# Kernel tuning notes

Measured on AMD Instinct MI355X. Metric: run time of the kernel, lower is better.

Reference implementation:

```python
import jax, jax.numpy as jnp
import numpy as np

N = 100000
E = 1600000
D = 128      # input_dim == hidden_dim
C = 40       # output_dim
L = 3        # num_layers
EPS = 1e-12  # F.normalize eps


def setup_inputs() -> dict:
    key = jax.random.key(0)
    ks = jax.random.split(key, 8)
    x = jax.random.normal(ks[0], (N, D), dtype=jnp.float32)
    edge_index = jax.random.randint(ks[1], (2, E), 0, N, dtype=jnp.int64)
    s = 1.0 / np.sqrt(D)
    # SAGEConv: lin_l (neighbor path, with bias), lin_r (root path, no bias)
    Wl = jax.random.uniform(ks[2], (L, D, D), jnp.float32, -s, s)
    bl = jax.random.uniform(ks[3], (L, D), jnp.float32, -s, s)
    Wr = jax.random.uniform(ks[4], (L, D, D), jnp.float32, -s, s)
    Wlin = jax.random.uniform(ks[5], (C, D), jnp.float32, -s, s)
    blin = jax.random.uniform(ks[6], (C,), jnp.float32, -s, s)
    return {"x": x, "edge_index": edge_index, "Wl": Wl, "bl": bl,
            "Wr": Wr, "Wlin": Wlin, "blin": blin}


def reference(x, edge_index, Wl, bl, Wr, Wlin, blin):
    src, dst = edge_index[0], edge_index[1]
    # in-degree counts for mean aggregation (computed once, reused per layer)
    cnt = jax.ops.segment_sum(jnp.ones((E,), jnp.float32), dst, num_segments=N)
    inv_cnt = (1.0 / jnp.maximum(cnt, 1.0))[:, None]  # [N,1]
    z = x
    for i in range(L):
        msg = z[src]  # gather [E, D]
        agg = jax.ops.segment_sum(msg, dst, num_segments=N) * inv_cnt  # mean [N, D]
        out = agg @ Wl[i].T + bl[i] + z @ Wr[i].T
        # SAGEConv normalize=True: L2 normalize per node
        nrm = jnp.linalg.norm(out, axis=-1, keepdims=True)
        out = out / jnp.maximum(nrm, EPS)
        z = jax.nn.relu(out)  # dropout p=0 -> identity
    return z @ Wlin.T + blin  # [N, C]
```

## Files before the change

kernel.cpp:

```cpp
#include <hip/hip_runtime.h>


typedef __bf16 bf16x8 __attribute__((ext_vector_type(8)));
typedef float  f32x4  __attribute__((ext_vector_type(4)));

#define MFMA16(a, b, c) __builtin_amdgcn_mfma_f32_16x16x32_bf16((a), (b), (c), 0, 0, 0)

__device__ __forceinline__ unsigned rne_bf16(float f) {
  unsigned u = __float_as_uint(f);
  unsigned r = u + 0x7FFFu + ((u >> 16) & 1u);
  return r >> 16;
}

__device__ __forceinline__ float bf_lo(unsigned u) { return __uint_as_float(u << 16); }
__device__ __forceinline__ float bf_hi(unsigned u) { return __uint_as_float(u & 0xFFFF0000u); }


__global__ __launch_bounds__(256) void histA_k(const int* __restrict__ dst,
                                               int* __restrict__ ghist, int E) {
  __shared__ int h[128];
  const int tid = threadIdx.x;
  if (tid < 128) h[tid] = 0;
  __syncthreads();
  const int e0 = blockIdx.x * 2048;
#pragma unroll
  for (int j = 0; j < 8; ++j) {
    int e = e0 + j * 256 + tid;
    if (e < E) atomicAdd(&h[dst[e] >> 10], 1);
  }
  __syncthreads();
  if (tid < 128 && h[tid]) atomicAdd(&ghist[tid], h[tid]);
}

__global__ void cscan_k(const int* __restrict__ ghist, int* __restrict__ cbase,
                        int* __restrict__ gcur, int E) {
  __shared__ int sd[128];
  const int tid = threadIdx.x;
  int v = ghist[tid];
  sd[tid] = v;
  __syncthreads();
  for (int off = 1; off < 128; off <<= 1) {
    int u = (tid >= off) ? sd[tid - off] : 0;
    __syncthreads();
    sd[tid] += u;
    __syncthreads();
  }
  int excl = sd[tid] - v;
  cbase[tid] = excl;
  gcur[tid] = excl;
  if (tid == 127) cbase[128] = sd[127];
}

__global__ __launch_bounds__(256) void bucketA_k(
    const int* __restrict__ src, const int* __restrict__ dst,
    int* __restrict__ gcur, unsigned* __restrict__ coarse, int E, int nc) {
  __shared__ int hist[128];
  __shared__ int sd[128];
  __shared__ int lpos[128];
  __shared__ int gbase[128];
  __shared__ unsigned stage[2048];
  __shared__ unsigned char sbuck[2048];

  const int tid = threadIdx.x;
  const int e0 = blockIdx.x * 2048;

  if (tid < 128) hist[tid] = 0;
  __syncthreads();

  int bv[8], pk[8];
#pragma unroll
  for (int j = 0; j < 8; ++j) {
    int e = e0 + j * 256 + tid;
    bv[j] = -1;
    if (e < E) {
      int s = src[e], d = dst[e];
      bv[j] = d >> 10;
      pk[j] = s | ((d & 1023) << 17);
      atomicAdd(&hist[bv[j]], 1);
    }
  }
  __syncthreads();

  if (tid < 128) sd[tid] = hist[tid];
  __syncthreads();
  for (int off = 1; off < 128; off <<= 1) {
    int t = 0;
    if (tid < 128 && tid >= off) t = sd[tid - off];
    __syncthreads();
    if (tid < 128) sd[tid] += t;
    __syncthreads();
  }
  if (tid < 128) {
    int excl = sd[tid] - hist[tid];
    lpos[tid] = excl;
    gbase[tid] = (tid < nc && hist[tid] > 0) ? atomicAdd(&gcur[tid], hist[tid]) : 0;
  }
  __syncthreads();

#pragma unroll
  for (int j = 0; j < 8; ++j) {
    if (bv[j] >= 0) {
      int slot = atomicAdd(&lpos[bv[j]], 1);
      stage[slot] = (unsigned)pk[j];
      sbuck[slot] = (unsigned char)bv[j];
    }
  }
  __syncthreads();

  const int total = sd[127];
  for (int i = tid; i < total; i += 256) {
    int b = sbuck[i];
    int excl = sd[b] - hist[b];
    coarse[gbase[b] + (i - excl)] = stage[i];
  }
}

__global__ __launch_bounds__(256) void bucketB_k(
    const int* __restrict__ cbase, const unsigned* __restrict__ coarse,
    int* __restrict__ esrc, int* __restrict__ offsets,
    float* __restrict__ inv_cnt, int n, int E) {
  __shared__ int hcnt[1024];
  __shared__ int cur[1024];
  __shared__ int sd[256];

  const int tid = threadIdx.x;
  const int b = blockIdx.x;
  const int base = b * 1024;
  const int nn = (n - base < 1024) ? (n - base) : 1024;
  const int cbeg = cbase[b];
  const int cend = cbase[b + 1];

  for (int j = tid; j < 1024; j += 256) hcnt[j] = 0;
  __syncthreads();
  for (int idx = cbeg + tid; idx < cend; idx += 256)
    atomicAdd(&hcnt[coarse[idx] >> 17], 1);
  __syncthreads();

  int b0 = hcnt[tid * 4], b1 = hcnt[tid * 4 + 1];
  int b2 = hcnt[tid * 4 + 2], b3 = hcnt[tid * 4 + 3];
  int tot = b0 + b1 + b2 + b3;
  sd[tid] = tot;
  __syncthreads();
  for (int off = 1; off < 256; off <<= 1) {
    int u = (tid >= off) ? sd[tid - off] : 0;
    __syncthreads();
    sd[tid] += u;
    __syncthreads();
  }
  int excl = cbeg + sd[tid] - tot;
  cur[tid * 4]     = excl;
  cur[tid * 4 + 1] = excl + b0;
  cur[tid * 4 + 2] = excl + b0 + b1;
  cur[tid * 4 + 3] = excl + b0 + b1 + b2;
  __syncthreads();

  for (int j = tid; j < nn; j += 256) {
    offsets[base + j] = cur[j];
    int c = hcnt[j] > 1 ? hcnt[j] : 1;
    inv_cnt[base + j] = 1.0f / (float)c;
  }
  if (tid == 0 && base + nn >= n) offsets[n] = cend;
  __syncthreads();

  for (int idx = cbeg + tid; idx < cend; idx += 256) {
    unsigned p = coarse[idx];
    int pos = atomicAdd(&cur[p >> 17], 1);
    esrc[pos] = (int)(p & 0x1FFFFu);
  }
}

__global__ void to_bf16_k(const float4* __restrict__ in, uint2* __restrict__ out, int n4) {
  int i = blockIdx.x * 256 + threadIdx.x;
  if (i >= n4) return;
  float4 f = in[i];
  uint2 o;
  o.x = rne_bf16(f.x) | (rne_bf16(f.y) << 16);
  o.y = rne_bf16(f.z) | (rne_bf16(f.w) << 16);
  out[i] = o;
}

__global__ void wfrag_prep_k(const float* __restrict__ Wl, const float* __restrict__ Wr,
                             unsigned short* __restrict__ wfrag) {
  int id = blockIdx.x * 256 + threadIdx.x;
  if (id >= 3 * 2 * 8 * 8 * 64) return;
  int l = id & 63;
  int c = (id >> 6) & 7;
  int t = (id >> 9) & 7;
  int p = (id >> 12) & 1;
  int layer = id >> 13;
  int col = t * 16 + (l & 15);
  int kbase = c * 32 + (l >> 4) * 8;
  unsigned short* dst = wfrag + (size_t)layer * 65536 +
                        ((((size_t)p * 8 + t) * 8 + c) * 64 + l) * 8;
#pragma unroll
  for (int j = 0; j < 8; ++j) {
    int k = kbase + j;
    float w = (k < 128) ? Wl[layer * 16384 + col * 128 + k]
                        : Wr[layer * 16384 + col * 128 + (k - 128)];
    unsigned h = rne_bf16(w);
    unsigned o;
    if (p == 0) o = h;
    else o = rne_bf16(w - __uint_as_float(h << 16));
    dst[j] = (unsigned short)o;
  }
}

__global__ void wlin_frag_k(const float* __restrict__ Wlin, unsigned short* __restrict__ wlf) {
  int id = blockIdx.x * 256 + threadIdx.x;
  if (id >= 3 * 4 * 64) return;
  int l = id & 63;
  int c = (id >> 6) & 3;
  int t = id >> 8;
  int col = t * 16 + (l & 15);
  int kbase = c * 32 + (l >> 4) * 8;
  unsigned short* dst = wlf + (size_t)id * 8;
#pragma unroll
  for (int j = 0; j < 8; ++j) {
    float w = (col < 40) ? Wlin[col * 128 + kbase + j] : 0.f;
    dst[j] = (unsigned short)rne_bf16(w);
  }
}

__global__ void aggregate_k(const unsigned short* __restrict__ zb,
                            const int* __restrict__ offsets,
                            const int* __restrict__ esrc,
                            const float* __restrict__ inv_cnt,
                            unsigned short* __restrict__ aggh,
                            unsigned short* __restrict__ aggl, int n) {
  int node = (blockIdx.x * 256 + threadIdx.x) >> 4;
  int l16 = threadIdx.x & 15;
  if (node >= n) return;
  int beg = offsets[node], end = offsets[node + 1];
  float a0 = 0.f, a1 = 0.f, a2 = 0.f, a3 = 0.f;
  float a4 = 0.f, a5 = 0.f, a6 = 0.f, a7 = 0.f;
  int t = beg;
  for (; t + 4 <= end; t += 4) {
    int s0 = esrc[t], s1 = esrc[t + 1], s2 = esrc[t + 2], s3 = esrc[t + 3];
    uint4 d0 = *(const uint4*)(zb + (size_t)s0 * 128 + l16 * 8);
    uint4 d1 = *(const uint4*)(zb + (size_t)s1 * 128 + l16 * 8);
    uint4 d2 = *(const uint4*)(zb + (size_t)s2 * 128 + l16 * 8);
    uint4 d3 = *(const uint4*)(zb + (size_t)s3 * 128 + l16 * 8);
    a0 += bf_lo(d0.x); a1 += bf_hi(d0.x); a2 += bf_lo(d0.y); a3 += bf_hi(d0.y);
    a4 += bf_lo(d0.z); a5 += bf_hi(d0.z); a6 += bf_lo(d0.w); a7 += bf_hi(d0.w);
    a0 += bf_lo(d1.x); a1 += bf_hi(d1.x); a2 += bf_lo(d1.y); a3 += bf_hi(d1.y);
    a4 += bf_lo(d1.z); a5 += bf_hi(d1.z); a6 += bf_lo(d1.w); a7 += bf_hi(d1.w);
    a0 += bf_lo(d2.x); a1 += bf_hi(d2.x); a2 += bf_lo(d2.y); a3 += bf_hi(d2.y);
    a4 += bf_lo(d2.z); a5 += bf_hi(d2.z); a6 += bf_lo(d2.w); a7 += bf_hi(d2.w);
    a0 += bf_lo(d3.x); a1 += bf_hi(d3.x); a2 += bf_lo(d3.y); a3 += bf_hi(d3.y);
    a4 += bf_lo(d3.z); a5 += bf_hi(d3.z); a6 += bf_lo(d3.w); a7 += bf_hi(d3.w);
  }
  for (; t + 2 <= end; t += 2) {
    int s0 = esrc[t], s1 = esrc[t + 1];
    uint4 d0 = *(const uint4*)(zb + (size_t)s0 * 128 + l16 * 8);
    uint4 d1 = *(const uint4*)(zb + (size_t)s1 * 128 + l16 * 8);
    a0 += bf_lo(d0.x); a1 += bf_hi(d0.x); a2 += bf_lo(d0.y); a3 += bf_hi(d0.y);
    a4 += bf_lo(d0.z); a5 += bf_hi(d0.z); a6 += bf_lo(d0.w); a7 += bf_hi(d0.w);
    a0 += bf_lo(d1.x); a1 += bf_hi(d1.x); a2 += bf_lo(d1.y); a3 += bf_hi(d1.y);
    a4 += bf_lo(d1.z); a5 += bf_hi(d1.z); a6 += bf_lo(d1.w); a7 += bf_hi(d1.w);
  }
  if (t < end) {
    int s0 = esrc[t];
    uint4 d0 = *(const uint4*)(zb + (size_t)s0 * 128 + l16 * 8);
    a0 += bf_lo(d0.x); a1 += bf_hi(d0.x); a2 += bf_lo(d0.y); a3 += bf_hi(d0.y);
    a4 += bf_lo(d0.z); a5 += bf_hi(d0.z); a6 += bf_lo(d0.w); a7 += bf_hi(d0.w);
  }
  float ic = inv_cnt[node];
  a0 *= ic; a1 *= ic; a2 *= ic; a3 *= ic;
  a4 *= ic; a5 *= ic; a6 *= ic; a7 *= ic;
  unsigned h0 = rne_bf16(a0), h1 = rne_bf16(a1), h2 = rne_bf16(a2), h3 = rne_bf16(a3);
  unsigned h4 = rne_bf16(a4), h5 = rne_bf16(a5), h6 = rne_bf16(a6), h7 = rne_bf16(a7);
  uint4 hv, lv;
  hv.x = h0 | (h1 << 16); hv.y = h2 | (h3 << 16);
  hv.z = h4 | (h5 << 16); hv.w = h6 | (h7 << 16);
  lv.x = rne_bf16(a0 - __uint_as_float(h0 << 16)) | (rne_bf16(a1 - __uint_as_float(h1 << 16)) << 16);
  lv.y = rne_bf16(a2 - __uint_as_float(h2 << 16)) | (rne_bf16(a3 - __uint_as_float(h3 << 16)) << 16);
  lv.z = rne_bf16(a4 - __uint_as_float(h4 << 16)) | (rne_bf16(a5 - __uint_as_float(h5 << 16)) << 16);
  lv.w = rne_bf16(a6 - __uint_as_float(h6 << 16)) | (rne_bf16(a7 - __uint_as_float(h7 << 16)) << 16);
  *(uint4*)(aggh + (size_t)node * 128 + l16 * 8) = hv;
  *(uint4*)(aggl + (size_t)node * 128 + l16 * 8) = lv;
}

__global__ __launch_bounds__(256) void sage_layer_mfma_k(
    const unsigned short* __restrict__ zb,
    const unsigned short* __restrict__ aggh, const unsigned short* __restrict__ aggl,
    const unsigned short* __restrict__ wf, const float* __restrict__ bl,
    unsigned short* __restrict__ out_bf, int n, int ntiles) {
  __shared__ unsigned short Ah_s[32 * 256];
  __shared__ unsigned short Al_s[32 * 128];
  __shared__ float psum[2][4][16];

  const int lane = threadIdx.x & 63;
  const int wv = threadIdx.x >> 6;
  const int g = lane >> 4;
  const int rl = lane & 15;

  const bf16x8* wfv = (const bf16x8*)wf;
  const int t0 = wv * 2, t1 = wv * 2 + 1;
  bf16x8 Bh0[8], Bh1[8], Bl0[8], Bl1[8];
#pragma unroll
  for (int c = 0; c < 8; ++c) {
    Bh0[c] = wfv[((0 * 8 + t0) * 8 + c) * 64 + lane];
    Bh1[c] = wfv[((0 * 8 + t1) * 8 + c) * 64 + lane];
    Bl0[c] = wfv[((1 * 8 + t0) * 8 + c) * 64 + lane];
    Bl1[c] = wfv[((1 * 8 + t1) * 8 + c) * 64 + lane];
  }
  const float b0 = bl[t0 * 16 + rl];
  const float b1 = bl[t1 * 16 + rl];

  char* pAh = (char*)Ah_s;
  char* pAl = (char*)Al_s;

  for (int tile = blockIdx.x; tile < ntiles; tile += gridDim.x) {
    const int v0 = tile * 32;

#pragma unroll
    for (int q = 0; q < 2; ++q) {
      int lin = q * 2048 + threadIdx.x * 8;
      int r = lin >> 7;
      int col = lin & 127;
      int v = v0 + r; v = (v < n) ? v : (n - 1);
      int swz = (r & 7) << 4;
      uint4 dh = *(const uint4*)(aggh + (size_t)v * 128 + col);
      uint4 dz = *(const uint4*)(zb + (size_t)v * 128 + col);
      uint4 dl = *(const uint4*)(aggl + (size_t)v * 128 + col);
      *(uint4*)(pAh + ((r * 512 + col * 2) ^ swz)) = dh;
      *(uint4*)(pAh + ((r * 512 + 256 + col * 2) ^ swz)) = dz;
      *(uint4*)(pAl + ((r * 256 + col * 2) ^ swz)) = dl;
    }
    __syncthreads();

#pragma unroll
    for (int s = 0; s < 2; ++s) {
      f32x4 a0 = {0.f, 0.f, 0.f, 0.f};
      f32x4 a1 = {0.f, 0.f, 0.f, 0.f};
      const int rowH = (s * 16 + rl) * 512;
      const int rowL = (s * 16 + rl) * 256;
      const int swz = (rl & 7) << 4;
#pragma unroll
      for (int c = 0; c < 4; ++c) {
        int offH = (rowH + c * 64 + g * 16) ^ swz;
        int offL = (rowL + c * 64 + g * 16) ^ swz;
        bf16x8 ah = *(const bf16x8*)(pAh + offH);
        bf16x8 al = *(const bf16x8*)(pAl + offL);
        a0 = MFMA16(ah, Bh0[c], a0); a1 = MFMA16(ah, Bh1[c], a1);
        a0 = MFMA16(ah, Bl0[c], a0); a1 = MFMA16(ah, Bl1[c], a1);
        a0 = MFMA16(al, Bh0[c], a0); a1 = MFMA16(al, Bh1[c], a1);
      }
#pragma unroll
      for (int c = 4; c < 8; ++c) {
        int offH = (rowH + c * 64 + g * 16) ^ swz;
        bf16x8 ah = *(const bf16x8*)(pAh + offH);
        a0 = MFMA16(ah, Bh0[c], a0); a1 = MFMA16(ah, Bh1[c], a1);
        a0 = MFMA16(ah, Bl0[c], a0); a1 = MFMA16(ah, Bl1[c], a1);
      }
      float pr[4];
#pragma unroll
      for (int j = 0; j < 4; ++j) {
        a0[j] += b0; a1[j] += b1;
        pr[j] = a0[j] * a0[j] + a1[j] * a1[j];
      }
#pragma unroll
      for (int m = 1; m < 16; m <<= 1) {
#pragma unroll
        for (int j = 0; j < 4; ++j) pr[j] += __shfl_xor(pr[j], m);
      }
      if (rl == 0) {
#pragma unroll
        for (int j = 0; j < 4; ++j) psum[s][wv][g * 4 + j] = pr[j];
      }
      __syncthreads();
#pragma unroll
      for (int j = 0; j < 4; ++j) {
        int row16 = g * 4 + j;
        float tot = psum[s][0][row16] + psum[s][1][row16] +
                    psum[s][2][row16] + psum[s][3][row16];
        float inv = 1.0f / fmaxf(sqrtf(tot), 1e-12f);
        int v = v0 + s * 16 + row16;
        if (v < n) {
          float o0 = fmaxf(a0[j] * inv, 0.f);
          float o1 = fmaxf(a1[j] * inv, 0.f);
          out_bf[(size_t)v * 128 + t0 * 16 + rl] = (unsigned short)rne_bf16(o0);
          out_bf[(size_t)v * 128 + t1 * 16 + rl] = (unsigned short)rne_bf16(o1);
        }
      }
    }
    __syncthreads();
  }
}

__global__ __launch_bounds__(256, 4) void final_linear_mfma_k(
    const unsigned short* __restrict__ zb, const unsigned short* __restrict__ wlf,
    const float* __restrict__ blin, float* __restrict__ out, int n, int ntiles) {
  __shared__ unsigned short Az[64 * 128];

  const int lane = threadIdx.x & 63;
  const int wv = threadIdx.x >> 6;
  const int g = lane >> 4;
  const int rl = lane & 15;

  const bf16x8* wv8 = (const bf16x8*)wlf;
  bf16x8 B[3][4];
#pragma unroll
  for (int t = 0; t < 3; ++t)
#pragma unroll
    for (int c = 0; c < 4; ++c) B[t][c] = wv8[(t * 4 + c) * 64 + lane];
  float bias[3];
#pragma unroll
  for (int t = 0; t < 3; ++t) {
    int col = t * 16 + rl;
    bias[t] = (col < 40) ? blin[col] : 0.f;
  }

  char* pAz = (char*)Az;

  for (int tile = blockIdx.x; tile < ntiles; tile += gridDim.x) {
    const int v0 = tile * 64;
#pragma unroll
    for (int q = 0; q < 4; ++q) {
      int lin = q * 2048 + threadIdx.x * 8;
      int r = lin >> 7;
      int col = lin & 127;
      int v = v0 + r; v = (v < n) ? v : (n - 1);
      uint4 d = *(const uint4*)(zb + (size_t)v * 128 + col);
      int byte = (r * 256 + col * 2) ^ ((r & 7) << 4);
      *(uint4*)(pAz + byte) = d;
    }
    __syncthreads();

    f32x4 acc0 = {0.f, 0.f, 0.f, 0.f};
    f32x4 acc1 = {0.f, 0.f, 0.f, 0.f};
    f32x4 acc2 = {0.f, 0.f, 0.f, 0.f};
    const int rowB = (wv * 16 + rl) * 256;
    const int swz = (rl & 7) << 4;
#pragma unroll
    for (int c = 0; c < 4; ++c) {
      int off = (rowB + c * 64 + g * 16) ^ swz;
      bf16x8 a = *(const bf16x8*)(pAz + off);
      acc0 = MFMA16(a, B[0][c], acc0);
      acc1 = MFMA16(a, B[1][c], acc1);
      acc2 = MFMA16(a, B[2][c], acc2);
    }
#pragma unroll
    for (int j = 0; j < 4; ++j) {
      int v = v0 + wv * 16 + g * 4 + j;
      if (v < n) {
        float* op = out + (size_t)v * 40;
        op[rl] = acc0[j] + bias[0];
        op[16 + rl] = acc1[j] + bias[1];
        if (rl < 8) op[32 + rl] = acc2[j] + bias[2];
      }
    }
    __syncthreads();
  }
}


extern "C" void kernel_launch(void* const* d_in, const int* in_sizes, int n_in,
                              void* d_out, int out_size, void* d_ws, size_t ws_size,
                              hipStream_t stream) {
  const float* x    = (const float*)d_in[0];
  const int*   ei   = (const int*)d_in[1];
  const float* Wl   = (const float*)d_in[2];
  const float* bl   = (const float*)d_in[3];
  const float* Wr   = (const float*)d_in[4];
  const float* Wlin = (const float*)d_in[5];
  const float* blin = (const float*)d_in[6];

  const int N = in_sizes[0] / 128;
  const int E = in_sizes[1] / 2;
  const int D = 128;
  const int NC = (N + 1023) >> 10;

  const int* src = ei;
  const int* dstp = ei + E;

  unsigned short* planeA = (unsigned short*)d_ws;
  unsigned short* planeB = planeA + (size_t)N * D;
  unsigned short* aggh   = planeB + (size_t)N * D;
  unsigned short* aggl   = aggh + (size_t)N * D;
  float* inv_cnt = (float*)(aggl + (size_t)N * D);
  unsigned short* wlf = (unsigned short*)(inv_cnt + N);
  unsigned short* Wfrag = wlf + 6144;
  int*   offsets = (int*)(Wfrag + 3 * 65536);
  int*   esrc    = offsets + N + 1;
  unsigned* coarse = (unsigned*)(esrc + E);
  int*   cbase   = (int*)(coarse + E);
  int*   gcur    = cbase + 129;
  int*   ghist   = gcur + 128;

  hipMemsetAsync(ghist, 0, 128 * 4, stream);
  histA_k<<<(E + 2047) / 2048, 256, 0, stream>>>(dstp, ghist, E);
  cscan_k<<<1, 128, 0, stream>>>(ghist, cbase, gcur, E);
  bucketA_k<<<(E + 2047) / 2048, 256, 0, stream>>>(src, dstp, gcur, coarse, E, NC);
  bucketB_k<<<NC, 256, 0, stream>>>(cbase, coarse, esrc, offsets, inv_cnt, N, E);

  wfrag_prep_k<<<96, 256, 0, stream>>>(Wl, Wr, Wfrag);
  wlin_frag_k<<<3, 256, 0, stream>>>(Wlin, wlf);
  to_bf16_k<<<((N * 32) + 255) / 256, 256, 0, stream>>>((const float4*)x, (uint2*)planeA, N * 32);

  const int aggGrid = (N * 16 + 255) / 256;
  const int ntiles = (N + 31) / 32;

  aggregate_k<<<aggGrid, 256, 0, stream>>>(planeA, offsets, esrc, inv_cnt, aggh, aggl, N);
  sage_layer_mfma_k<<<ntiles, 256, 0, stream>>>(planeA, aggh, aggl, Wfrag + 0 * 65536, bl + 0 * D, planeB, N, ntiles);
  aggregate_k<<<aggGrid, 256, 0, stream>>>(planeB, offsets, esrc, inv_cnt, aggh, aggl, N);
  sage_layer_mfma_k<<<ntiles, 256, 0, stream>>>(planeB, aggh, aggl, Wfrag + 1 * 65536, bl + 1 * D, planeA, N, ntiles);
  aggregate_k<<<aggGrid, 256, 0, stream>>>(planeA, offsets, esrc, inv_cnt, aggh, aggl, N);
  sage_layer_mfma_k<<<ntiles, 256, 0, stream>>>(planeA, aggh, aggl, Wfrag + 2 * 65536, bl + 2 * D, planeB, N, ntiles);

  const int ntiles64 = (N + 63) / 64;
  final_linear_mfma_k<<<ntiles64, 256, 0, stream>>>(planeB, wlf, blin, (float*)d_out, N, ntiles64);
}
```

Baseline: 425.7 us.

## Drop low-part aggregate split and replace histogram pass with fixed-capacity buckets

The aggregate kernel now stores only a single bf16 copy of the mean-aggregated features, no longer a hi/lo pair. This removes one N×128 write per layer, the matching tile load, and a third of the MFMAs on the aggregate half of the layer GEMM, at the cost of aggregate precision. The CSR build also drops the separate histogram pass. Coarse buckets now write into fixed-capacity slots (average plus 4096 slack) and the prefix scan runs afterward on the fill counters. A bucket holding more edges than the slack allows would overflow into its neighbour.

```diff
diff --git a/kernel.cpp b/kernel.cpp
--- a/kernel.cpp
+++ b/kernel.cpp
@@ -16,39 +16,8 @@
 __device__ __forceinline__ float bf_hi(unsigned u) { return __uint_as_float(u & 0xFFFF0000u); }
 
 
-__global__ __launch_bounds__(256) void histA_k(const int* __restrict__ dst,
-                                               int* __restrict__ ghist, int E) {
-  __shared__ int h[128];
-  const int tid = threadIdx.x;
-  if (tid < 128) h[tid] = 0;
-  __syncthreads();
-  const int e0 = blockIdx.x * 2048;
-#pragma unroll
-  for (int j = 0; j < 8; ++j) {
-    int e = e0 + j * 256 + tid;
-    if (e < E) atomicAdd(&h[dst[e] >> 10], 1);
-  }
-  __syncthreads();
-  if (tid < 128 && h[tid]) atomicAdd(&ghist[tid], h[tid]);
-}
-
-__global__ void cscan_k(const int* __restrict__ ghist, int* __restrict__ cbase,
-                        int* __restrict__ gcur, int E) {
-  __shared__ int sd[128];
-  const int tid = threadIdx.x;
-  int v = ghist[tid];
-  sd[tid] = v;
-  __syncthreads();
-  for (int off = 1; off < 128; off <<= 1) {
-    int u = (tid >= off) ? sd[tid - off] : 0;
-    __syncthreads();
-    sd[tid] += u;
-    __syncthreads();
-  }
-  int excl = sd[tid] - v;
-  cbase[tid] = excl;
-  gcur[tid] = excl;
-  if (tid == 127) cbase[128] = sd[127];
+__global__ void gcur_init_k(int* __restrict__ gcur, int cap) {
+  gcur[threadIdx.x] = threadIdx.x * cap;
 }
 
 __global__ __launch_bounds__(256) void bucketA_k(
@@ -115,10 +84,28 @@
   }
 }
 
+__global__ void cscan_k(const int* __restrict__ gcur, int cap, int nc,
+                        int* __restrict__ cbase) {
+  __shared__ int sd[128];
+  const int tid = threadIdx.x;
+  int v = (tid < nc) ? (gcur[tid] - tid * cap) : 0;
+  sd[tid] = v;
+  __syncthreads();
+  for (int off = 1; off < 128; off <<= 1) {
+    int u = (tid >= off) ? sd[tid - off] : 0;
+    __syncthreads();
+    sd[tid] += u;
+    __syncthreads();
+  }
+  cbase[tid] = sd[tid] - v;
+  if (tid == 127) cbase[128] = sd[127];
+}
+
 __global__ __launch_bounds__(256) void bucketB_k(
-    const int* __restrict__ cbase, const unsigned* __restrict__ coarse,
+    const int* __restrict__ cbase, const int* __restrict__ gcur,
+    const unsigned* __restrict__ coarse, int cap,
     int* __restrict__ esrc, int* __restrict__ offsets,
-    float* __restrict__ inv_cnt, int n, int E) {
+    float* __restrict__ inv_cnt, int n) {
   __shared__ int hcnt[1024];
   __shared__ int cur[1024];
   __shared__ int sd[256];
@@ -127,12 +114,13 @@
   const int b = blockIdx.x;
   const int base = b * 1024;
   const int nn = (n - base < 1024) ? (n - base) : 1024;
-  const int cbeg = cbase[b];
-  const int cend = cbase[b + 1];
+  const int wbeg = b * cap;
+  const int wend = gcur[b];
+  const int gdst = cbase[b];
 
   for (int j = tid; j < 1024; j += 256) hcnt[j] = 0;
   __syncthreads();
-  for (int idx = cbeg + tid; idx < cend; idx += 256)
+  for (int idx = wbeg + tid; idx < wend; idx += 256)
     atomicAdd(&hcnt[coarse[idx] >> 17], 1);
   __syncthreads();
 
@@ -147,7 +135,7 @@
     sd[tid] += u;
     __syncthreads();
   }
-  int excl = cbeg + sd[tid] - tot;
+  int excl = gdst + sd[tid] - tot;
   cur[tid * 4]     = excl;
   cur[tid * 4 + 1] = excl + b0;
   cur[tid * 4 + 2] = excl + b0 + b1;
@@ -159,10 +147,10 @@
     int c = hcnt[j] > 1 ? hcnt[j] : 1;
     inv_cnt[base + j] = 1.0f / (float)c;
   }
-  if (tid == 0 && base + nn >= n) offsets[n] = cend;
-  __syncthreads();
-
-  for (int idx = cbeg + tid; idx < cend; idx += 256) {
+  if (tid == 0 && base + nn >= n) offsets[n] = gdst + (wend - wbeg);
+  __syncthreads();
+
+  for (int idx = wbeg + tid; idx < wend; idx += 256) {
     unsigned p = coarse[idx];
     int pos = atomicAdd(&cur[p >> 17], 1);
     esrc[pos] = (int)(p & 0x1FFFFu);
@@ -225,8 +213,7 @@
                             const int* __restrict__ offsets,
                             const int* __restrict__ esrc,
                             const float* __restrict__ inv_cnt,
-                            unsigned short* __restrict__ aggh,
-                            unsigned short* __restrict__ aggl, int n) {
+                            unsigned short* __restrict__ aggh, int n) {
   int node = (blockIdx.x * 256 + threadIdx.x) >> 4;
   int l16 = threadIdx.x & 15;
   if (node >= n) return;
@@ -265,28 +252,19 @@
     a4 += bf_lo(d0.z); a5 += bf_hi(d0.z); a6 += bf_lo(d0.w); a7 += bf_hi(d0.w);
   }
   float ic = inv_cnt[node];
-  a0 *= ic; a1 *= ic; a2 *= ic; a3 *= ic;
-  a4 *= ic; a5 *= ic; a6 *= ic; a7 *= ic;
-  unsigned h0 = rne_bf16(a0), h1 = rne_bf16(a1), h2 = rne_bf16(a2), h3 = rne_bf16(a3);
-  unsigned h4 = rne_bf16(a4), h5 = rne_bf16(a5), h6 = rne_bf16(a6), h7 = rne_bf16(a7);
-  uint4 hv, lv;
-  hv.x = h0 | (h1 << 16); hv.y = h2 | (h3 << 16);
-  hv.z = h4 | (h5 << 16); hv.w = h6 | (h7 << 16);
-  lv.x = rne_bf16(a0 - __uint_as_float(h0 << 16)) | (rne_bf16(a1 - __uint_as_float(h1 << 16)) << 16);
-  lv.y = rne_bf16(a2 - __uint_as_float(h2 << 16)) | (rne_bf16(a3 - __uint_as_float(h3 << 16)) << 16);
-  lv.z = rne_bf16(a4 - __uint_as_float(h4 << 16)) | (rne_bf16(a5 - __uint_as_float(h5 << 16)) << 16);
-  lv.w = rne_bf16(a6 - __uint_as_float(h6 << 16)) | (rne_bf16(a7 - __uint_as_float(h7 << 16)) << 16);
+  uint4 hv;
+  hv.x = rne_bf16(a0 * ic) | (rne_bf16(a1 * ic) << 16);
+  hv.y = rne_bf16(a2 * ic) | (rne_bf16(a3 * ic) << 16);
+  hv.z = rne_bf16(a4 * ic) | (rne_bf16(a5 * ic) << 16);
+  hv.w = rne_bf16(a6 * ic) | (rne_bf16(a7 * ic) << 16);
   *(uint4*)(aggh + (size_t)node * 128 + l16 * 8) = hv;
-  *(uint4*)(aggl + (size_t)node * 128 + l16 * 8) = lv;
 }
 
 __global__ __launch_bounds__(256) void sage_layer_mfma_k(
-    const unsigned short* __restrict__ zb,
-    const unsigned short* __restrict__ aggh, const unsigned short* __restrict__ aggl,
+    const unsigned short* __restrict__ zb, const unsigned short* __restrict__ aggh,
     const unsigned short* __restrict__ wf, const float* __restrict__ bl,
     unsigned short* __restrict__ out_bf, int n, int ntiles) {
   __shared__ unsigned short Ah_s[32 * 256];
-  __shared__ unsigned short Al_s[32 * 128];
   __shared__ float psum[2][4][16];
 
   const int lane = threadIdx.x & 63;
@@ -308,7 +286,6 @@
   const float b1 = bl[t1 * 16 + rl];
 
   char* pAh = (char*)Ah_s;
-  char* pAl = (char*)Al_s;
 
   for (int tile = blockIdx.x; tile < ntiles; tile += gridDim.x) {
     const int v0 = tile * 32;
@@ -322,10 +299,8 @@
       int swz = (r & 7) << 4;
       uint4 dh = *(const uint4*)(aggh + (size_t)v * 128 + col);
       uint4 dz = *(const uint4*)(zb + (size_t)v * 128 + col);
-      uint4 dl = *(const uint4*)(aggl + (size_t)v * 128 + col);
       *(uint4*)(pAh + ((r * 512 + col * 2) ^ swz)) = dh;
       *(uint4*)(pAh + ((r * 512 + 256 + col * 2) ^ swz)) = dz;
-      *(uint4*)(pAl + ((r * 256 + col * 2) ^ swz)) = dl;
     }
     __syncthreads();
 
@@ -334,20 +309,9 @@
       f32x4 a0 = {0.f, 0.f, 0.f, 0.f};
       f32x4 a1 = {0.f, 0.f, 0.f, 0.f};
       const int rowH = (s * 16 + rl) * 512;
-      const int rowL = (s * 16 + rl) * 256;
       const int swz = (rl & 7) << 4;
 #pragma unroll
-      for (int c = 0; c < 4; ++c) {
-        int offH = (rowH + c * 64 + g * 16) ^ swz;
-        int offL = (rowL + c * 64 + g * 16) ^ swz;
-        bf16x8 ah = *(const bf16x8*)(pAh + offH);
-        bf16x8 al = *(const bf16x8*)(pAl + offL);
-        a0 = MFMA16(ah, Bh0[c], a0); a1 = MFMA16(ah, Bh1[c], a1);
-        a0 = MFMA16(ah, Bl0[c], a0); a1 = MFMA16(ah, Bl1[c], a1);
-        a0 = MFMA16(al, Bh0[c], a0); a1 = MFMA16(al, Bh1[c], a1);
-      }
-#pragma unroll
-      for (int c = 4; c < 8; ++c) {
+      for (int c = 0; c < 8; ++c) {
         int offH = (rowH + c * 64 + g * 16) ^ swz;
         bf16x8 ah = *(const bf16x8*)(pAh + offH);
         a0 = MFMA16(ah, Bh0[c], a0); a1 = MFMA16(ah, Bh1[c], a1);
@@ -470,6 +434,7 @@
   const int E = in_sizes[1] / 2;
   const int D = 128;
   const int NC = (N + 1023) >> 10;
+  const int cap = (E + NC - 1) / NC + 4096;
 
   const int* src = ei;
   const int* dstp = ei + E;
@@ -477,22 +442,19 @@
   unsigned short* planeA = (unsigned short*)d_ws;
   unsigned short* planeB = planeA + (size_t)N * D;
   unsigned short* aggh   = planeB + (size_t)N * D;
-  unsigned short* aggl   = aggh + (size_t)N * D;
-  float* inv_cnt = (float*)(aggl + (size_t)N * D);
+  float* inv_cnt = (float*)(aggh + (size_t)N * D);
   unsigned short* wlf = (unsigned short*)(inv_cnt + N);
   unsigned short* Wfrag = wlf + 6144;
   int*   offsets = (int*)(Wfrag + 3 * 65536);
   int*   esrc    = offsets + N + 1;
   unsigned* coarse = (unsigned*)(esrc + E);
-  int*   cbase   = (int*)(coarse + E);
+  int*   cbase   = (int*)(coarse + (size_t)NC * cap);
   int*   gcur    = cbase + 129;
-  int*   ghist   = gcur + 128;
-
-  hipMemsetAsync(ghist, 0, 128 * 4, stream);
-  histA_k<<<(E + 2047) / 2048, 256, 0, stream>>>(dstp, ghist, E);
-  cscan_k<<<1, 128, 0, stream>>>(ghist, cbase, gcur, E);
+
+  gcur_init_k<<<1, 128, 0, stream>>>(gcur, cap);
   bucketA_k<<<(E + 2047) / 2048, 256, 0, stream>>>(src, dstp, gcur, coarse, E, NC);
-  bucketB_k<<<NC, 256, 0, stream>>>(cbase, coarse, esrc, offsets, inv_cnt, N, E);
+  cscan_k<<<1, 128, 0, stream>>>(gcur, cap, NC, cbase);
+  bucketB_k<<<NC, 256, 0, stream>>>(cbase, gcur, coarse, cap, esrc, offsets, inv_cnt, N);
 
   wfrag_prep_k<<<96, 256, 0, stream>>>(Wl, Wr, Wfrag);
   wlin_frag_k<<<3, 256, 0, stream>>>(Wlin, wlf);
@@ -501,12 +463,12 @@
   const int aggGrid = (N * 16 + 255) / 256;
   const int ntiles = (N + 31) / 32;
 
-  aggregate_k<<<aggGrid, 256, 0, stream>>>(planeA, offsets, esrc, inv_cnt, aggh, aggl, N);
-  sage_layer_mfma_k<<<ntiles, 256, 0, stream>>>(planeA, aggh, aggl, Wfrag + 0 * 65536, bl + 0 * D, planeB, N, ntiles);
-  aggregate_k<<<aggGrid, 256, 0, stream>>>(planeB, offsets, esrc, inv_cnt, aggh, aggl, N);
-  sage_layer_mfma_k<<<ntiles, 256, 0, stream>>>(planeB, aggh, aggl, Wfrag + 1 * 65536, bl + 1 * D, planeA, N, ntiles);
-  aggregate_k<<<aggGrid, 256, 0, stream>>>(planeA, offsets, esrc, inv_cnt, aggh, aggl, N);
-  sage_layer_mfma_k<<<ntiles, 256, 0, stream>>>(planeA, aggh, aggl, Wfrag + 2 * 65536, bl + 2 * D, planeB, N, ntiles);
+  aggregate_k<<<aggGrid, 256, 0, stream>>>(planeA, offsets, esrc, inv_cnt, aggh, N);
+  sage_layer_mfma_k<<<ntiles, 256, 0, stream>>>(planeA, aggh, Wfrag + 0 * 65536, bl + 0 * D, planeB, N, ntiles);
+  aggregate_k<<<aggGrid, 256, 0, stream>>>(planeB, offsets, esrc, inv_cnt, aggh, N);
+  sage_layer_mfma_k<<<ntiles, 256, 0, stream>>>(planeB, aggh, Wfrag + 1 * 65536, bl + 1 * D, planeA, N, ntiles);
+  aggregate_k<<<aggGrid, 256, 0, stream>>>(planeA, offsets, esrc, inv_cnt, aggh, N);
+  sage_layer_mfma_k<<<ntiles, 256, 0, stream>>>(planeA, aggh, Wfrag + 2 * 65536, bl + 2 * D, planeB, N, ntiles);
 
   const int ntiles64 = (N + 63) / 64;
   final_linear_mfma_k<<<ntiles64, 256, 0, stream>>>(planeB, wlf, blin, (float*)d_out, N, ntiles64);
```

After: 376.4 us. 1.13x faster.
